# Kernel optimization log

Hardware: AMD Instinct MI355X
Metric: run time of the kernel (lower is better)

The kernel has to match this reference:

```python
import jax, jax.numpy as jnp
import numpy as np

NEG_FILL = -9e15   # matches -9000000000000000.0 in the torch source
ALPHA = 0.2        # LeakyReLU negative slope
N, F_IN, F_OUT = 8192, 94, 16


def setup_inputs() -> dict:
    key = jax.random.key(0)
    k1, k2, k3, k4 = jax.random.split(key, 4)
    h = jax.random.normal(k1, (N, F_IN), dtype=jnp.float32)
    adj = jax.random.randint(k2, (N, N), 0, 2, dtype=jnp.int32)
    # learned params: W (Linear in->out, no bias) and attn vector (2*F_OUT, 1)
    W = jax.random.normal(k3, (F_IN, F_OUT), dtype=jnp.float32) * (1.0 / np.sqrt(F_IN))
    attn = jax.random.normal(k4, (2 * F_OUT, 1), dtype=jnp.float32) * 0.3
    return {"h": h, "adj": adj, "W": W, "attn": attn}


def reference(h, adj, W, attn):
    # Wh: [N, F_OUT]
    Wh = h @ W
    # cat(Wh_i, Wh_j) @ attn == Wh_i @ a1 + Wh_j @ a2 : avoids the N x N x 2F concat
    a1 = attn[:F_OUT, 0]   # [F_OUT]
    a2 = attn[F_OUT:, 0]   # [F_OUT]
    s_src = Wh @ a1        # [N] contribution of node i (row)
    s_dst = Wh @ a2        # [N] contribution of node j (col)
    e = jax.nn.leaky_relu(s_src[:, None] + s_dst[None, :], negative_slope=ALPHA)  # [N, N]
    att = jnp.where(adj > 0, e, NEG_FILL)
    att = jax.nn.softmax(att, axis=1)          # row-wise over neighbors
    # dropout is identity in eval mode
    h_prime = att @ Wh                         # [N, F_OUT]
    return jax.nn.elu(h_prime)
```

## Files before the change

### kernel.cpp

```cpp
#include <hip/hip_runtime.h>
#include <hip/hip_bf16.h>
#include <math.h>

#define N      8192
#define FIN    94
#define FOUT   16
#define ALPHA  0.2f
#define BM     64
#define JCH    1024
#define NCH    (N / JCH)
#define NRB    (N / BM)
#define NT_T   (JCH / 32)

#define AR_OFF 65536
#define CR_OFF (AR_OFF + N)
#define BX_OFF (AR_OFF + 2*N)
#define DX_OFF (AR_OFF + 3*N)
#define PN_OFF (AR_OFF + 4*N)
#define PL_OFF (PN_OFF + NCH*N*FOUT)

typedef int   i32x4 __attribute__((ext_vector_type(4)));
typedef float f32x4 __attribute__((ext_vector_type(4)));
typedef short s16x8 __attribute__((ext_vector_type(8)));

__global__ __launch_bounds__(256) void wh_score_kernel(
    const float* __restrict__ h, const float* __restrict__ W,
    const float* __restrict__ attn, float* __restrict__ ws)
{
    const int gid = blockIdx.x * 256 + threadIdx.x;
    const int i = gid >> 4;
    const int k = gid & 15;
    const float* hrow = h + i * FIN;
    float a0 = 0.f, a1 = 0.f, a2 = 0.f, a3 = 0.f;
    #pragma unroll
    for (int c = 0; c < 92; c += 4) {
        a0 = fmaf(hrow[c],     W[c * FOUT + k],       a0);
        a1 = fmaf(hrow[c + 1], W[(c + 1) * FOUT + k], a1);
        a2 = fmaf(hrow[c + 2], W[(c + 2) * FOUT + k], a2);
        a3 = fmaf(hrow[c + 3], W[(c + 3) * FOUT + k], a3);
    }
    a0 = fmaf(hrow[92], W[92 * FOUT + k], a0);
    a1 = fmaf(hrow[93], W[93 * FOUT + k], a1);
    const float acc = (a0 + a1) + (a2 + a3);

    __hip_bfloat16* whtb = (__hip_bfloat16*)ws;
    whtb[k * N + i] = __float2bfloat16(acc);

    float ps = acc * attn[k];
    float pd = acc * attn[FOUT + k];
    #pragma unroll
    for (int mk = 1; mk < 16; mk <<= 1) {
        ps += __shfl_xor(ps, mk);
        pd += __shfl_xor(pd, mk);
    }
    if (k == 0) {
        ws[AR_OFF + i] = __expf(ps);
        ws[CR_OFF + i] = __expf(ALPHA * ps);
        ws[BX_OFF + i] = __expf(pd);
        ws[DX_OFF + i] = __expf(ALPHA * pd);
    }
}

__global__ __launch_bounds__(256, 4) void gat_mfma_kernel(
    const int* __restrict__ adj, const float* __restrict__ ws,
    float* __restrict__ wso)
{
    __shared__ float Bl[JCH];
    __shared__ float Dl[JCH];

    const int tid = threadIdx.x;
    const int rb = blockIdx.x & (NRB - 1);
    const int ch = blockIdx.x >> 7;
    const int i0 = rb * BM;
    const int jc0 = ch * JCH;

    {
        const int t4 = tid * 4;
        *(f32x4*)(Bl + t4) = *(const f32x4*)(ws + BX_OFF + jc0 + t4);
        *(f32x4*)(Dl + t4) = *(const f32x4*)(ws + DX_OFF + jc0 + t4);
    }
    __syncthreads();

    const int w    = tid >> 6;
    const int lane = tid & 63;
    const int c15  = lane & 15;
    const int g    = lane >> 4;
    const int arow = i0 + w * 16 + c15;

    const float Ar = ws[AR_OFF + arow];
    const float Cr = ws[CR_OFF + arow];

    const unsigned short* __restrict__ whtb = (const unsigned short*)ws;
    const int* __restrict__ ap            = adj + (size_t)arow * N + jc0 + 8 * g;
    const unsigned short* __restrict__ wp = whtb + c15 * N + jc0 + 8 * g;

    f32x4 acc = {0.f, 0.f, 0.f, 0.f};
    float lsum = 0.f;

    i32x4 a0_0, a1_0, a0_1, a1_1, a0_2, a1_2, a0_3, a1_3;
    s16x8 fb_0, fb_1, fb_2, fb_3;

#define ISSUE(s, t) do {                                                       \
    const int off_ = 32 * (t);                                                 \
    a0_##s = *(const i32x4*)(ap + off_);                                       \
    a1_##s = *(const i32x4*)(ap + off_ + 4);                                   \
    fb_##s = *(const s16x8*)(wp + off_);                                       \
} while (0)

#define COMPUTE(s, t) do {                                                     \
    const int lb = (t) * 32 + 8 * g;                                           \
    const f32x4 B0 = *(const f32x4*)(Bl + lb);                                 \
    const f32x4 B1 = *(const f32x4*)(Bl + lb + 4);                             \
    const f32x4 D0 = *(const f32x4*)(Dl + lb);                                 \
    const f32x4 D1 = *(const f32x4*)(Dl + lb + 4);                             \
    float wf[8];                                                               \
    _Pragma("unroll") for (int e = 0; e < 4; ++e) {                            \
        const float ww = (a0_##s[e] > 0) ?                                     \
            fmaxf(Ar * B0[e], Cr * D0[e]) : 0.0f;                              \
        wf[e] = ww; lsum += ww;                                                \
    }                                                                          \
    _Pragma("unroll") for (int e = 0; e < 4; ++e) {                            \
        const float ww = (a1_##s[e] > 0) ?                                     \
            fmaxf(Ar * B1[e], Cr * D1[e]) : 0.0f;                              \
        wf[4 + e] = ww; lsum += ww;                                            \
    }                                                                          \
    s16x8 fa;                                                                  \
    _Pragma("unroll") for (int e = 0; e < 8; ++e)                              \
        fa[e] = (short)__builtin_bit_cast(unsigned short,                      \
                                          __float2bfloat16(wf[e]));           \
    acc = __builtin_amdgcn_mfma_f32_16x16x32_bf16(fa, fb_##s, acc, 0, 0, 0);   \
} while (0)

    ISSUE(0, 0); ISSUE(1, 1); ISSUE(2, 2); ISSUE(3, 3);

    #pragma unroll 1
    for (int t = 0; t < NT_T - 4; t += 4) {
        COMPUTE(0, t);     ISSUE(0, t + 4);
        COMPUTE(1, t + 1); ISSUE(1, t + 5);
        COMPUTE(2, t + 2); ISSUE(2, t + 6);
        COMPUTE(3, t + 3); ISSUE(3, t + 7);
    }
    COMPUTE(0, NT_T - 4); COMPUTE(1, NT_T - 3);
    COMPUTE(2, NT_T - 2); COMPUTE(3, NT_T - 1);
#undef ISSUE
#undef COMPUTE

    lsum += __shfl_xor(lsum, 16);
    lsum += __shfl_xor(lsum, 32);

    #pragma unroll
    for (int r = 0; r < 4; ++r) {
        const int grow = i0 + w * 16 + 4 * g + r;
        wso[PN_OFF + ((size_t)ch * N + grow) * FOUT + c15] = acc[r];
    }
    if (g == 0)
        wso[PL_OFF + ch * N + arow] = lsum;
}

__global__ __launch_bounds__(256) void reduce_kernel(
    const float* __restrict__ ws, float* __restrict__ out)
{
    const int gid = blockIdx.x * 256 + threadIdx.x;
    const int i = gid >> 4;
    float num = 0.f, den = 0.f;
    #pragma unroll
    for (int ch = 0; ch < NCH; ++ch) {
        num += ws[PN_OFF + (size_t)ch * (N * FOUT) + gid];
        den += ws[PL_OFF + ch * N + i];
    }
    const float v = num / den;
    out[gid] = (v > 0.0f) ? v : expm1f(v);
}

extern "C" void kernel_launch(void* const* d_in, const int* in_sizes, int n_in,
                              void* d_out, int out_size, void* d_ws, size_t ws_size,
                              hipStream_t stream)
{
    const float* h    = (const float*)d_in[0];
    const int*   adj  = (const int*)d_in[1];
    const float* W    = (const float*)d_in[2];
    const float* attn = (const float*)d_in[3];
    float* out = (float*)d_out;
    float* ws  = (float*)d_ws;

    wh_score_kernel<<<(N * FOUT) / 256, 256, 0, stream>>>(h, W, attn, ws);
    gat_mfma_kernel<<<NRB * NCH, 256, 0, stream>>>(adj, ws, ws);
    reduce_kernel<<<(N * FOUT) / 256, 256, 0, stream>>>(ws, out);
}
```

Baseline: 58.98 us.

## Fuse chunk reduction into attention kernel with per-block full-row split across waves

Each block now handles 16 rows across all 8192 columns, with 8 waves each covering a 1024-column slice. Partial numerators and denominators are combined in shared memory and the ELU output is written directly, so the separate reduce kernel and its workspace round trip go away. The cost is a 64KB shared buffer per block holding the full B/D score vectors, which may limit occupancy. The block count also drops to 512, and only one wave does the final reduction.

```diff
diff --git a/kernel.cpp b/kernel.cpp
--- a/kernel.cpp
+++ b/kernel.cpp
@@ -6,18 +6,15 @@
 #define FIN    94
 #define FOUT   16
 #define ALPHA  0.2f
-#define BM     64
-#define JCH    1024
-#define NCH    (N / JCH)
-#define NRB    (N / BM)
-#define NT_T   (JCH / 32)
+#define BM     16
+#define WJ     1024
+#define NWAVE  8
+#define NT_T   (WJ / 32)
 
 #define AR_OFF 65536
 #define CR_OFF (AR_OFF + N)
 #define BX_OFF (AR_OFF + 2*N)
 #define DX_OFF (AR_OFF + 3*N)
-#define PN_OFF (AR_OFF + 4*N)
-#define PL_OFF (PN_OFF + NCH*N*FOUT)
 
 typedef int   i32x4 __attribute__((ext_vector_type(4)));
 typedef float f32x4 __attribute__((ext_vector_type(4)));
@@ -61,23 +58,20 @@
     }
 }
 
-__global__ __launch_bounds__(256, 4) void gat_mfma_kernel(
+__global__ __launch_bounds__(512, 4) void gat_mfma_kernel(
     const int* __restrict__ adj, const float* __restrict__ ws,
-    float* __restrict__ wso)
+    float* __restrict__ out)
 {
-    __shared__ float Bl[JCH];
-    __shared__ float Dl[JCH];
+    __shared__ float smem[16384];
 
     const int tid = threadIdx.x;
-    const int rb = blockIdx.x & (NRB - 1);
-    const int ch = blockIdx.x >> 7;
-    const int i0 = rb * BM;
-    const int jc0 = ch * JCH;
+    const int i0 = blockIdx.x * BM;
 
-    {
-        const int t4 = tid * 4;
-        *(f32x4*)(Bl + t4) = *(const f32x4*)(ws + BX_OFF + jc0 + t4);
-        *(f32x4*)(Dl + t4) = *(const f32x4*)(ws + DX_OFF + jc0 + t4);
+    #pragma unroll
+    for (int u = 0; u < 4; ++u) {
+        const int idx = u * 2048 + tid * 4;
+        *(f32x4*)(smem + idx)        = *(const f32x4*)(ws + BX_OFF + idx);
+        *(f32x4*)(smem + 8192 + idx) = *(const f32x4*)(ws + DX_OFF + idx);
     }
     __syncthreads();
 
@@ -85,11 +79,14 @@
     const int lane = tid & 63;
     const int c15  = lane & 15;
     const int g    = lane >> 4;
-    const int arow = i0 + w * 16 + c15;
+    const int arow = i0 + c15;
+    const int jc0  = w * WJ;
 
     const float Ar = ws[AR_OFF + arow];
     const float Cr = ws[CR_OFF + arow];
 
+    const float* __restrict__ Bl = smem + jc0;
+    const float* __restrict__ Dl = smem + 8192 + jc0;
     const unsigned short* __restrict__ whtb = (const unsigned short*)ws;
     const int* __restrict__ ap            = adj + (size_t)arow * N + jc0 + 8 * g;
     const unsigned short* __restrict__ wp = whtb + c15 * N + jc0 + 8 * g;
@@ -148,28 +145,32 @@
     lsum += __shfl_xor(lsum, 16);
     lsum += __shfl_xor(lsum, 32);
 
+    __syncthreads();
     #pragma unroll
-    for (int r = 0; r < 4; ++r) {
-        const int grow = i0 + w * 16 + 4 * g + r;
-        wso[PN_OFF + ((size_t)ch * N + grow) * FOUT + c15] = acc[r];
+    for (int r = 0; r < 4; ++r)
+        smem[(w * 64 + lane) * 4 + r] = acc[r];
+    if (g == 0)
+        smem[2048 + w * 16 + c15] = lsum;
+    __syncthreads();
+
+    if (w == 0) {
+        float tot[4] = {0.f, 0.f, 0.f, 0.f};
+        float den[4] = {0.f, 0.f, 0.f, 0.f};
+        #pragma unroll
+        for (int ww = 0; ww < NWAVE; ++ww) {
+            #pragma unroll
+            for (int r = 0; r < 4; ++r) {
+                tot[r] += smem[(ww * 64 + lane) * 4 + r];
+                den[r] += smem[2048 + ww * 16 + (4 * g + r)];
+            }
+        }
+        #pragma unroll
+        for (int r = 0; r < 4; ++r) {
+            const float v = tot[r] / den[r];
+            out[(i0 + 4 * g + r) * FOUT + c15] =
+                (v > 0.0f) ? v : expm1f(v);
+        }
     }
-    if (g == 0)
-        wso[PL_OFF + ch * N + arow] = lsum;
-}
-
-__global__ __launch_bounds__(256) void reduce_kernel(
-    const float* __restrict__ ws, float* __restrict__ out)
-{
-    const int gid = blockIdx.x * 256 + threadIdx.x;
-    const int i = gid >> 4;
-    float num = 0.f, den = 0.f;
-    #pragma unroll
-    for (int ch = 0; ch < NCH; ++ch) {
-        num += ws[PN_OFF + (size_t)ch * (N * FOUT) + gid];
-        den += ws[PL_OFF + ch * N + i];
-    }
-    const float v = num / den;
-    out[gid] = (v > 0.0f) ? v : expm1f(v);
 }
 
 extern "C" void kernel_launch(void* const* d_in, const int* in_sizes, int n_in,
@@ -184,6 +185,5 @@
     float* ws  = (float*)d_ws;
 
     wh_score_kernel<<<(N * FOUT) / 256, 256, 0, stream>>>(h, W, attn, ws);
-    gat_mfma_kernel<<<NRB * NCH, 256, 0, stream>>>(adj, ws, ws);
-    reduce_kernel<<<(N * FOUT) / 256, 256, 0, stream>>>(ws, out);
+    gat_mfma_kernel<<<N / BM, 512, 0, stream>>>(adj, ws, out);
 }
```

After: 59.33 us. No clear change (+0.6%).
